# Optimization experiments

Measured on AMD Instinct MI355X. Metric: run time of the kernel, lower is better.

Reference implementation:

```python
import jax, jax.numpy as jnp
import numpy as np

N_NODES = 100000
N_EDGES = 400000
N_GRAPHS = 5000
F_IN = 64
H = 128
OUT = 1
N_LAYERS = 3  # gat_conv + 2 atom_gats
NEG_SLOPE = 0.01


def _gat_conv(x_src, x_dst, src, dst, W, a_src, a_dst, b, num_dst):
    """PyG GATConv, heads=1, add_self_loops=False, negative_slope=0.01.

    x_src: [Ns, Fin], x_dst: [Nd, Fin]; src/dst: [E] int; W: [Fin, H];
    a_src, a_dst, b: [H]. Returns [Nd, H].
    """
    hs = x_src @ W                      # [Ns, H]
    hd = x_dst @ W                      # [Nd, H]
    as_n = hs @ a_src                   # [Ns]
    ad_n = hd @ a_dst                   # [Nd]
    e = jax.nn.leaky_relu(as_n[src] + ad_n[dst], NEG_SLOPE)  # [E]
    # segment softmax over destination nodes
    seg_max = jax.ops.segment_max(e, dst, num_segments=num_dst)
    seg_max = jnp.where(jnp.isfinite(seg_max), seg_max, 0.0)
    ex = jnp.exp(e - seg_max[dst])
    denom = jax.ops.segment_sum(ex, dst, num_segments=num_dst) + 1e-16
    alpha = ex / denom[dst]             # [E]
    out = jax.ops.segment_sum(alpha[:, None] * hs[src], dst, num_segments=num_dst)
    return out + b


def setup_inputs() -> dict:
    key = jax.random.key(0)
    ks = jax.random.split(key, 16)
    x = jax.random.normal(ks[0], (N_NODES, F_IN), dtype=jnp.float32)
    edge_index = jax.random.randint(ks[1], (2, N_EDGES), 0, N_NODES, dtype=jnp.int64)
    batch = jnp.sort(jax.random.randint(ks[2], (N_NODES,), 0, N_GRAPHS, dtype=jnp.int64))
    s_in = 1.0 / np.sqrt(F_IN)
    s_h = 1.0 / np.sqrt(H)
    W1 = jax.random.uniform(ks[3], (F_IN, H), jnp.float32, -s_in, s_in)
    b1 = jax.random.uniform(ks[4], (H,), jnp.float32, -s_in, s_in)
    gW = jax.random.normal(ks[5], (N_LAYERS, H, H), jnp.float32) * s_h
    g_asrc = jax.random.normal(ks[6], (N_LAYERS, H), jnp.float32) * s_h
    g_adst = jax.random.normal(ks[7], (N_LAYERS, H), jnp.float32) * s_h
    g_b = jnp.zeros((N_LAYERS, H), jnp.float32)
    mW = jax.random.normal(ks[8], (H, H), jnp.float32) * s_h
    m_asrc = jax.random.normal(ks[9], (H,), jnp.float32) * s_h
    m_adst = jax.random.normal(ks[10], (H,), jnp.float32) * s_h
    m_b = jnp.zeros((H,), jnp.float32)
    W2 = jax.random.uniform(ks[11], (H, OUT), jnp.float32, -s_h, s_h)
    b2 = jax.random.uniform(ks[12], (OUT,), jnp.float32, -s_h, s_h)
    return {"x": x, "edge_index": edge_index, "batch": batch,
            "W1": W1, "b1": b1, "gW": gW, "g_asrc": g_asrc,
            "g_adst": g_adst, "g_b": g_b, "mW": mW, "m_asrc": m_asrc,
            "m_adst": m_adst, "m_b": m_b, "W2": W2, "b2": b2}


def reference(x, edge_index, batch, W1, b1, gW, g_asrc, g_adst, g_b,
              mW, m_asrc, m_adst, m_b, W2, b2):
    src, dst = edge_index[0], edge_index[1]
    h = jax.nn.leaky_relu(x @ W1 + b1, NEG_SLOPE)            # lin1 + leaky_relu_
    for i in range(N_LAYERS):                                 # gat_conv + atom_gats
        h = jax.nn.elu(_gat_conv(h, h, src, dst, gW[i], g_asrc[i],
                                 g_adst[i], g_b[i], N_NODES))
    # global readout: node -> graph bipartite GAT
    pooled = jax.nn.relu(jax.ops.segment_sum(h, batch, num_segments=N_GRAPHS))
    row = jnp.arange(N_NODES)
    out = jax.nn.elu(_gat_conv(h, pooled, row, batch, mW, m_asrc,
                               m_adst, m_b, N_GRAPHS))
    return out @ W2 + b2                                      # [N_GRAPHS, OUT]
```

## Files before the change

### kernel.cpp

```cpp
#include <hip/hip_runtime.h>
#include <hip/hip_fp16.h>
#include <math.h>
#include <stdint.h>

#define DEV __device__ __forceinline__

using f32x4 = __attribute__((ext_vector_type(4))) float;
using half8 = __attribute__((ext_vector_type(8))) _Float16;
typedef union { uint4 u; half8 h; } u4h8;

DEV float lrelu(float x){ return x > 0.f ? x : 0.01f*x; }
DEV float elu1(float x){ return x > 0.f ? x : __expf(x)-1.f; }

DEV int lower_bound_i(const int* __restrict__ a, int n, int key){
  int lo = 0, hi = n;
  while (lo < hi){ int mid = (lo+hi)>>1; if (a[mid] < key) lo = mid+1; else hi = mid; }
  return lo;
}

DEV void wsplit(float v, unsigned short* __restrict__ H, unsigned short* __restrict__ L, size_t o){
  __half h = __float2half_rn(v);
  float lo = (v - __half2float(h)) * 1024.f;
  H[o] = __half_as_ushort(h);
  L[o] = __half_as_ushort(__float2half_rn(lo));
}

__global__ void wprep_all(const float* __restrict__ W1, const float* __restrict__ gW,
    const float* __restrict__ mW,
    unsigned short* __restrict__ w1h, unsigned short* __restrict__ w1l,
    unsigned short* __restrict__ gwh, unsigned short* __restrict__ gwl,
    unsigned short* __restrict__ mwh, unsigned short* __restrict__ mwl,
    int* __restrict__ deg, unsigned long long* __restrict__ bstat,
    int* __restrict__ bctr, int Nn, int nG, int nscan)
{
  int i = blockIdx.x*256 + threadIdx.x;
  if (i < Nn) deg[i] = 0;
  if (i < nscan) bstat[i] = 0ull;
  if (i == 0) *bctr = 0;
  if (i < 8192){
    int k = i >> 7, n = i & 127;
    wsplit(W1[i], w1h, w1l, (size_t)n*64 + k);
  }
  if (i < nG){
    int mat = i >> 14; int rem = i & 16383;
    int k = rem >> 7, n = rem & 127;
    wsplit(gW[i], gwh, gwl, (size_t)mat*16384 + (size_t)n*128 + k);
  }
  if (i < 16384){
    int k = i >> 7, n = i & 127;
    wsplit(mW[i], mwh, mwl, (size_t)n*128 + k);
  }
}

__global__ __launch_bounds__(256, 3) void gemm_lin1(
    const float* __restrict__ X, const unsigned short* __restrict__ Wt_hi,
    const unsigned short* __restrict__ Wt_lo, const float* __restrict__ bias,
    unsigned short* __restrict__ Ch, int M)
{
  const int tid = threadIdx.x;
  const int lane = tid & 63;
  const int wv = tid >> 6;
  const int ml = lane & 15;
  const int kg = lane >> 4;
  const int R0 = blockIdx.x * 64;

  __shared__ uint32_t sA[2][1024];
  __shared__ float sC[4][32][36];

  const unsigned short* bhp[2];
  const unsigned short* blp[2];
  #pragma unroll
  for (int nt = 0; nt < 2; ++nt){
    int n = wv*32 + nt*16 + ml;
    bhp[nt] = Wt_hi + (size_t)n*64 + kg*8;
    blp[nt] = Wt_lo + (size_t)n*64 + kg*8;
  }

  {
    int row = tid >> 2, kq = tid & 3;
    int gr = R0 + row; gr = gr < M ? gr : M-1;
    const float4* xp = (const float4*)(X + (size_t)gr*64 + kq*16);
    int sub = kq >> 1;
    #pragma unroll
    for (int i = 0; i < 4; ++i){
      float4 v = xp[i];
      __half2 h0 = __floats2half2_rn(v.x, v.y);
      __half2 h1 = __floats2half2_rn(v.z, v.w);
      int slot = (kq & 1)*2 + (i >> 1);
      int slot_s = slot ^ ((row >> 1) & 3);
      int byte = row*64 + slot_s*16 + (i & 1)*8;
      *(uint2*)((char*)&sA[sub][0] + byte) = make_uint2(*(uint32_t*)&h0, *(uint32_t*)&h1);
    }
  }
  __syncthreads();

  f32x4 accH[4][2], accL[4][2];
  #pragma unroll
  for (int mt = 0; mt < 4; ++mt)
    #pragma unroll
    for (int nt = 0; nt < 2; ++nt){
      accH[mt][nt] = (f32x4){0.f,0.f,0.f,0.f};
      accL[mt][nt] = (f32x4){0.f,0.f,0.f,0.f};
    }

  #pragma unroll
  for (int sc = 0; sc < 2; ++sc){
    u4h8 bh[2], bl[2];
    #pragma unroll
    for (int nt = 0; nt < 2; ++nt){
      bh[nt].u = *(const uint4*)(bhp[nt] + sc*32);
      bl[nt].u = *(const uint4*)(blp[nt] + sc*32);
    }
    const char* buf = (const char*)&sA[sc][0];
    #pragma unroll
    for (int mt = 0; mt < 4; ++mt){
      int row = mt*16 + ml;
      int ba = row*64 + ((kg ^ ((row >> 1) & 3)) * 16);
      u4h8 A_;
      A_.u = *(const uint4*)(buf + ba);
      #pragma unroll
      for (int nt = 0; nt < 2; ++nt){
        accH[mt][nt] = __builtin_amdgcn_mfma_f32_16x16x32_f16(A_.h, bh[nt].h, accH[mt][nt], 0, 0, 0);
        accL[mt][nt] = __builtin_amdgcn_mfma_f32_16x16x32_f16(A_.h, bl[nt].h, accL[mt][nt], 0, 0, 0);
      }
    }
  }

  float bv[2] = { bias[wv*32 + ml], bias[wv*32 + 16 + ml] };
  #pragma unroll
  for (int p = 0; p < 2; ++p){
    #pragma unroll
    for (int mh = 0; mh < 2; ++mh){
      int mt = p*2 + mh;
      #pragma unroll
      for (int nt = 0; nt < 2; ++nt){
        #pragma unroll
        for (int r = 0; r < 4; ++r){
          float v = accH[mt][nt][r] + accL[mt][nt][r] * 9.765625e-4f;
          v = lrelu(v + bv[nt]);
          sC[wv][mh*16 + kg*4 + r][nt*16 + ml] = v;
        }
      }
    }
    __syncthreads();
    #pragma unroll
    for (int j = 0; j < 4; ++j){
      int row_l = j*8 + (lane >> 3);
      int c4 = (lane & 7) * 4;
      int grow = R0 + p*32 + row_l;
      if (grow < M){
        float4 v = *(const float4*)&sC[wv][row_l][c4];
        int gcol = wv*32 + c4;
        __half2 h0 = __floats2half2_rn(v.x, v.y);
        __half2 h1 = __floats2half2_rn(v.z, v.w);
        *(uint2*)(Ch + (size_t)grow*128 + gcol) = make_uint2(*(uint32_t*)&h0, *(uint32_t*)&h1);
      }
    }
    __syncthreads();
  }
}

template<int OUTMODE, bool DOTA, bool DOTB>
__global__ __launch_bounds__(256, 3) void gemm_mfma(
    const unsigned short* __restrict__ Ah, const unsigned short* __restrict__ Wt_hi,
    const unsigned short* __restrict__ Wt_lo,
    const float* __restrict__ va, const float* __restrict__ vb,
    unsigned short* __restrict__ Ch,
    float* __restrict__ outa, float* __restrict__ outb, int M)
{
  constexpr int K = 128;
  const int tid = threadIdx.x;
  const int lane = tid & 63;
  const int wv = tid >> 6;
  const int ml = lane & 15;
  const int kg = lane >> 4;
  const int R0 = blockIdx.x * 64;

  __shared__ uint32_t sA[4][1024];
  __shared__ float sC[4][32][36];
  __shared__ float sd[4][64][2];

  const unsigned short* bhp[2];
  const unsigned short* blp[2];
  #pragma unroll
  for (int nt = 0; nt < 2; ++nt){
    int n = wv*32 + nt*16 + ml;
    bhp[nt] = Wt_hi + (size_t)n*K + kg*8;
    blp[nt] = Wt_lo + (size_t)n*K + kg*8;
  }

  auto STAGE = [&](int ch){
    #pragma unroll
    for (int j = 0; j < 2; ++j){
      int sc = ch*2 + j;
      int o = tid*16;
      int row = o >> 6;
      int t = (o >> 4) & 3;
      int gr = R0 + row; gr = gr < M ? gr : M-1;
      int jj = t ^ ((row >> 1) & 3);
      const char* src = (const char*)(Ah + (size_t)gr*K + sc*32 + jj*8);
      char* dst = (char*)(&sA[(ch & 1)*2 + j][0]) + wv*1024;
      __builtin_amdgcn_global_load_lds(
          (const __attribute__((address_space(1))) void*)src,
          (__attribute__((address_space(3))) void*)dst, 16, 0, 0);
    }
  };

  f32x4 accH[4][2], accL[4][2];
  #pragma unroll
  for (int mt = 0; mt < 4; ++mt)
    #pragma unroll
    for (int nt = 0; nt < 2; ++nt){
      accH[mt][nt] = (f32x4){0.f,0.f,0.f,0.f};
      accL[mt][nt] = (f32x4){0.f,0.f,0.f,0.f};
    }

  STAGE(0);
  u4h8 bh[2][2], bl[2][2];
  #pragma unroll
  for (int j = 0; j < 2; ++j)
    #pragma unroll
    for (int nt = 0; nt < 2; ++nt){
      bh[j][nt].u = *(const uint4*)(bhp[nt] + j*32);
      bl[j][nt].u = *(const uint4*)(blp[nt] + j*32);
    }
  __syncthreads();

  #pragma unroll
  for (int ch = 0; ch < 2; ++ch){
    u4h8 bhN[2][2], blN[2][2];
    if (ch == 0){
      STAGE(1);
      #pragma unroll
      for (int j = 0; j < 2; ++j)
        #pragma unroll
        for (int nt = 0; nt < 2; ++nt){
          bhN[j][nt].u = *(const uint4*)(bhp[nt] + (2 + j)*32);
          blN[j][nt].u = *(const uint4*)(blp[nt] + (2 + j)*32);
        }
    }
    #pragma unroll
    for (int js = 0; js < 2; ++js){
      const char* buf = (const char*)&sA[(ch & 1)*2 + js][0];
      #pragma unroll
      for (int mt = 0; mt < 4; ++mt){
        int row = mt*16 + ml;
        int ba = row*64 + ((kg ^ ((row >> 1) & 3)) * 16);
        u4h8 A_;
        A_.u = *(const uint4*)(buf + ba);
        #pragma unroll
        for (int nt = 0; nt < 2; ++nt){
          accH[mt][nt] = __builtin_amdgcn_mfma_f32_16x16x32_f16(A_.h, bh[js][nt].h, accH[mt][nt], 0, 0, 0);
          accL[mt][nt] = __builtin_amdgcn_mfma_f32_16x16x32_f16(A_.h, bl[js][nt].h, accL[mt][nt], 0, 0, 0);
        }
      }
    }
    __syncthreads();
    if (ch == 0){
      #pragma unroll
      for (int j = 0; j < 2; ++j)
        #pragma unroll
        for (int nt = 0; nt < 2; ++nt){ bh[j][nt] = bhN[j][nt]; bl[j][nt] = blN[j][nt]; }
    }
  }

  #pragma unroll
  for (int mt = 0; mt < 4; ++mt)
    #pragma unroll
    for (int nt = 0; nt < 2; ++nt)
      accH[mt][nt] = accH[mt][nt] + accL[mt][nt] * 9.765625e-4f;

  if constexpr (DOTA || DOTB){
    float vaL[2] = {0.f,0.f}, vbL[2] = {0.f,0.f};
    if constexpr (DOTA){ vaL[0] = va[wv*32 + ml]; vaL[1] = va[wv*32 + 16 + ml]; }
    if constexpr (DOTB){ vbL[0] = vb[wv*32 + ml]; vbL[1] = vb[wv*32 + 16 + ml]; }
    #pragma unroll
    for (int mt = 0; mt < 4; ++mt){
      #pragma unroll
      for (int r = 0; r < 4; ++r){
        float pa = 0.f, pb = 0.f;
        #pragma unroll
        for (int nt = 0; nt < 2; ++nt){
          float v = accH[mt][nt][r];
          if constexpr (DOTA) pa = fmaf(v, vaL[nt], pa);
          if constexpr (DOTB) pb = fmaf(v, vbL[nt], pb);
        }
        #pragma unroll
        for (int o = 8; o; o >>= 1){
          if constexpr (DOTA) pa += __shfl_xor(pa, o, 64);
          if constexpr (DOTB) pb += __shfl_xor(pb, o, 64);
        }
        if (ml == 0){
          int rl = mt*16 + kg*4 + r;
          sd[wv][rl][0] = pa;
          sd[wv][rl][1] = pb;
        }
      }
    }
    __syncthreads();
    if (tid < 64){
      int row = R0 + tid;
      if (row < M){
        if constexpr (DOTA)
          outa[row] = sd[0][tid][0] + sd[1][tid][0] + sd[2][tid][0] + sd[3][tid][0];
        if constexpr (DOTB)
          outb[row] = sd[0][tid][1] + sd[1][tid][1] + sd[2][tid][1] + sd[3][tid][1];
      }
    }
  }

  if constexpr (OUTMODE == 2){
    if constexpr (DOTA || DOTB) __syncthreads();
    #pragma unroll
    for (int p = 0; p < 2; ++p){
      #pragma unroll
      for (int mh = 0; mh < 2; ++mh){
        int mt = p*2 + mh;
        #pragma unroll
        for (int nt = 0; nt < 2; ++nt){
          #pragma unroll
          for (int r = 0; r < 4; ++r)
            sC[wv][mh*16 + kg*4 + r][nt*16 + ml] = accH[mt][nt][r];
        }
      }
      __syncthreads();
      #pragma unroll
      for (int j = 0; j < 4; ++j){
        int row_l = j*8 + (lane >> 3);
        int c4 = (lane & 7) * 4;
        int grow = R0 + p*32 + row_l;
        if (grow < M){
          float4 v = *(const float4*)&sC[wv][row_l][c4];
          int gcol = wv*32 + c4;
          __half2 h0 = __floats2half2_rn(v.x, v.y);
          __half2 h1 = __floats2half2_rn(v.z, v.w);
          *(uint2*)(Ch + (size_t)grow*128 + gcol) = make_uint2(*(uint32_t*)&h0, *(uint32_t*)&h1);
        }
      }
      __syncthreads();
    }
  }
}

__global__ void hist_k(const int* __restrict__ dstv, int* __restrict__ deg, int E){
  int e = blockIdx.x*256 + threadIdx.x;
  if (e < E) atomicAdd(&deg[dstv[e]], 1);
}

__global__ void scan_onepass(const int* __restrict__ deg, int* __restrict__ rp,
    int* __restrict__ cur, unsigned long long* __restrict__ bstat,
    int* __restrict__ bctr, int n, int E)
{
  __shared__ int sbid;
  __shared__ int swsum[4];
  __shared__ int sprev;
  if (threadIdx.x == 0) sbid = atomicAdd(bctr, 1);
  __syncthreads();
  const int bid = sbid;
  int i = bid*256 + threadIdx.x;
  int lane = threadIdx.x & 63, wv = threadIdx.x >> 6;
  int v = (i < n) ? deg[i] : 0;
  int inc = v;
  #pragma unroll
  for (int o = 1; o < 64; o <<= 1){
    int u = __shfl_up(inc, o, 64);
    if (lane >= o) inc += u;
  }
  if (lane == 63) swsum[wv] = inc;
  __syncthreads();
  if (threadIdx.x == 0){
    int bsum = swsum[0]+swsum[1]+swsum[2]+swsum[3];
    atomicExch(&bstat[bid], (1ull << 62) | (unsigned long long)(unsigned)bsum);
    int prev = 0;
    for (int j = bid - 1; j >= 0; --j){
      unsigned long long s;
      do { s = atomicAdd(&bstat[j], 0ull); } while ((s >> 62) == 0);
      prev += (int)(s & 0xffffffffull);
      if ((s >> 62) == 2) break;
    }
    atomicExch(&bstat[bid], (2ull << 62) | (unsigned long long)(unsigned)(prev + bsum));
    sprev = prev;
  }
  __syncthreads();
  int woff = sprev;
  for (int wq = 0; wq < wv; ++wq) woff += swsum[wq];
  int excl = woff + inc - v;
  if (i < n){ rp[i] = excl; cur[i] = excl; }
  if (bid == 0 && threadIdx.x == 0) rp[n] = E;
}

__global__ void scatter_k(const int* __restrict__ srcv, const int* __restrict__ dstv,
                          int* __restrict__ cur, int* __restrict__ ssorted, int E){
  int e = blockIdx.x*256 + threadIdx.x;
  if (e < E){
    int p = atomicAdd(&cur[dstv[e]], 1);
    ssorted[p] = srcv[e];
  }
}

__global__ __launch_bounds__(256) void gat_agg(const int* __restrict__ ssorted,
    const int* __restrict__ rp,
    const float* __restrict__ asn, const float* __restrict__ adn,
    const uint4* __restrict__ hsv, const float* __restrict__ bias,
    uint4* __restrict__ outv, int Nn)
{
  const int lane = threadIdx.x & 63;
  const int wv = threadIdx.x >> 6;
  const int l16 = lane & 15;
  const int gbase = lane & 48;
  const int d = blockIdx.x*16 + wv*4 + (lane >> 4);
  const bool valid = d < Nn;
  const int dc = valid ? d : Nn-1;
  const int lo = rp[dc], hi = rp[dc+1];
  const int deg = valid ? (hi - lo) : 0;
  const float ad = adn[dc];
  float acc[8] = {0.f,0.f,0.f,0.f,0.f,0.f,0.f,0.f};

  const bool fast = (deg <= 16);
  const int fdeg = fast ? deg : 0;
  int mdeg = fdeg;
  mdeg = max(mdeg, __shfl_xor(mdeg, 16, 64));
  mdeg = max(mdeg, __shfl_xor(mdeg, 32, 64));

  int sid = 0; float lg = -1e30f;
  if (l16 < fdeg){
    sid = ssorted[lo + l16];
    lg = lrelu(asn[sid] + ad);
  }
  float m = lg;
  m = fmaxf(m, __shfl_xor(m, 8, 64));
  m = fmaxf(m, __shfl_xor(m, 4, 64));
  m = fmaxf(m, __shfl_xor(m, 2, 64));
  m = fmaxf(m, __shfl_xor(m, 1, 64));
  float p = (l16 < fdeg) ? __expf(lg - m) : 0.f;
  float s = p;
  s += __shfl_xor(s, 8, 64);
  s += __shfl_xor(s, 4, 64);
  s += __shfl_xor(s, 2, 64);
  s += __shfl_xor(s, 1, 64);
  float alpha = p * (1.f / (s + 1e-16f));

  for (int i = 0; i < mdeg; ++i){
    if (i < fdeg){
      float al = __shfl(alpha, gbase + i, 64);
      int sd = __shfl(sid, gbase + i, 64);
      uint4 v = hsv[(size_t)sd*16 + l16];
      float2 f0 = __half22float2(*(__half2*)&v.x);
      float2 f1 = __half22float2(*(__half2*)&v.y);
      float2 f2 = __half22float2(*(__half2*)&v.z);
      float2 f3 = __half22float2(*(__half2*)&v.w);
      acc[0] = fmaf(al, f0.x, acc[0]); acc[1] = fmaf(al, f0.y, acc[1]);
      acc[2] = fmaf(al, f1.x, acc[2]); acc[3] = fmaf(al, f1.y, acc[3]);
      acc[4] = fmaf(al, f2.x, acc[4]); acc[5] = fmaf(al, f2.y, acc[5]);
      acc[6] = fmaf(al, f3.x, acc[6]); acc[7] = fmaf(al, f3.y, acc[7]);
    }
  }

  if (!fast){
    float mg = -1e30f;
    for (int e = l16; e < deg; e += 16){
      int sd = ssorted[lo + e];
      mg = fmaxf(mg, lrelu(asn[sd] + ad));
    }
    mg = fmaxf(mg, __shfl_xor(mg, 8, 64));
    mg = fmaxf(mg, __shfl_xor(mg, 4, 64));
    mg = fmaxf(mg, __shfl_xor(mg, 2, 64));
    mg = fmaxf(mg, __shfl_xor(mg, 1, 64));
    float sg = 0.f;
    for (int e = l16; e < deg; e += 16){
      int sd = ssorted[lo + e];
      sg += __expf(lrelu(asn[sd] + ad) - mg);
    }
    sg += __shfl_xor(sg, 8, 64);
    sg += __shfl_xor(sg, 4, 64);
    sg += __shfl_xor(sg, 2, 64);
    sg += __shfl_xor(sg, 1, 64);
    float inv = 1.f / (sg + 1e-16f);
    for (int e = 0; e < deg; ++e){
      int sd = ssorted[lo + e];
      float a = __expf(lrelu(asn[sd] + ad) - mg) * inv;
      uint4 v = hsv[(size_t)sd*16 + l16];
      float2 f0 = __half22float2(*(__half2*)&v.x);
      float2 f1 = __half22float2(*(__half2*)&v.y);
      float2 f2 = __half22float2(*(__half2*)&v.z);
      float2 f3 = __half22float2(*(__half2*)&v.w);
      acc[0] = fmaf(a, f0.x, acc[0]); acc[1] = fmaf(a, f0.y, acc[1]);
      acc[2] = fmaf(a, f1.x, acc[2]); acc[3] = fmaf(a, f1.y, acc[3]);
      acc[4] = fmaf(a, f2.x, acc[4]); acc[5] = fmaf(a, f2.y, acc[5]);
      acc[6] = fmaf(a, f3.x, acc[6]); acc[7] = fmaf(a, f3.y, acc[7]);
    }
  }

  if (valid){
    float4 b0 = ((const float4*)bias)[l16*2];
    float4 b1 = ((const float4*)bias)[l16*2 + 1];
    __half2 h0 = __floats2half2_rn(elu1(acc[0]+b0.x), elu1(acc[1]+b0.y));
    __half2 h1 = __floats2half2_rn(elu1(acc[2]+b0.z), elu1(acc[3]+b0.w));
    __half2 h2 = __floats2half2_rn(elu1(acc[4]+b1.x), elu1(acc[5]+b1.y));
    __half2 h3 = __floats2half2_rn(elu1(acc[6]+b1.z), elu1(acc[7]+b1.w));
    outv[(size_t)d*16 + l16] = make_uint4(*(uint32_t*)&h0, *(uint32_t*)&h1,
                                          *(uint32_t*)&h2, *(uint32_t*)&h3);
  }
}

__global__ __launch_bounds__(256) void pool_relu(const uint4* __restrict__ hv,
    const int* __restrict__ batch, uint4* __restrict__ ptail, int Nn, int G)
{
  const int lane = threadIdx.x & 63;
  const int wv = threadIdx.x >> 6;
  const int l16 = lane & 15;
  const int g = blockIdx.x*16 + wv*4 + (lane >> 4);
  if (g >= G) return;
  const int lo = lower_bound_i(batch, Nn, g);
  const int hi = lower_bound_i(batch, Nn, g + 1);
  float acc[8] = {0.f,0.f,0.f,0.f,0.f,0.f,0.f,0.f};
  for (int i = lo; i < hi; ++i){
    uint4 v = hv[(size_t)i*16 + l16];
    float2 f0 = __half22float2(*(__half2*)&v.x);
    float2 f1 = __half22float2(*(__half2*)&v.y);
    float2 f2 = __half22float2(*(__half2*)&v.z);
    float2 f3 = __half22float2(*(__half2*)&v.w);
    acc[0] += f0.x; acc[1] += f0.y; acc[2] += f1.x; acc[3] += f1.y;
    acc[4] += f2.x; acc[5] += f2.y; acc[6] += f3.x; acc[7] += f3.y;
  }
  __half2 h0 = __floats2half2_rn(fmaxf(acc[0],0.f), fmaxf(acc[1],0.f));
  __half2 h1 = __floats2half2_rn(fmaxf(acc[2],0.f), fmaxf(acc[3],0.f));
  __half2 h2 = __floats2half2_rn(fmaxf(acc[4],0.f), fmaxf(acc[5],0.f));
  __half2 h3 = __floats2half2_rn(fmaxf(acc[6],0.f), fmaxf(acc[7],0.f));
  ptail[(size_t)g*16 + l16] = make_uint4(*(uint32_t*)&h0, *(uint32_t*)&h1,
                                         *(uint32_t*)&h2, *(uint32_t*)&h3);
}

__global__ __launch_bounds__(128) void mol_agg(const float* __restrict__ as2,
    const float* __restrict__ ad2, const unsigned short* __restrict__ hs2,
    const int* __restrict__ batch, const float* __restrict__ bias,
    const float* __restrict__ W2, const float* __restrict__ b2,
    float* __restrict__ out, int Nn)
{
  const int g = blockIdx.x;
  const int c = threadIdx.x;
  __shared__ int sb[2];
  __shared__ float red[2];
  if (c < 2) sb[c] = lower_bound_i(batch, Nn, g + c);
  __syncthreads();
  const int lo = sb[0], hi = sb[1];
  const float ad = ad2[g];

  float mt = -1e30f;
  for (int i = lo + c; i < hi; i += 128) mt = fmaxf(mt, lrelu(as2[i] + ad));
  #pragma unroll
  for (int o = 32; o; o >>= 1) mt = fmaxf(mt, __shfl_xor(mt, o, 64));
  if ((c & 63) == 0) red[c >> 6] = mt;
  __syncthreads();
  const float m = fmaxf(red[0], red[1]);

  float st = 0.f;
  for (int i = lo + c; i < hi; i += 128) st += __expf(lrelu(as2[i] + ad) - m);
  #pragma unroll
  for (int o = 32; o; o >>= 1) st += __shfl_xor(st, o, 64);
  __syncthreads();
  if ((c & 63) == 0) red[c >> 6] = st;
  __syncthreads();
  const float inv = 1.f / (red[0] + red[1] + 1e-16f);

  float acc = 0.f;
  for (int i = lo; i < hi; ++i){
    float wgt = __expf(lrelu(as2[i] + ad) - m) * inv;
    acc = fmaf(wgt, __half2float(__ushort_as_half(hs2[(size_t)i*128 + c])), acc);
  }
  float v = elu1(acc + bias[c]);

  float r = v * W2[c];
  #pragma unroll
  for (int o = 32; o; o >>= 1) r += __shfl_xor(r, o, 64);
  __syncthreads();
  if ((c & 63) == 0) red[c >> 6] = r;
  __syncthreads();
  if (c == 0) out[g] = red[0] + red[1] + b2[0];
}

extern "C" void kernel_launch(void* const* d_in, const int* in_sizes, int n_in,
                              void* d_out, int out_size, void* d_ws, size_t ws_size,
                              hipStream_t stream)
{
  const float* x      = (const float*)d_in[0];
  const int*   ei     = (const int*)  d_in[1];
  const int*   batch  = (const int*)  d_in[2];
  const float* W1     = (const float*)d_in[3];
  const float* b1     = (const float*)d_in[4];
  const float* gW     = (const float*)d_in[5];
  const float* g_asrc = (const float*)d_in[6];
  const float* g_adst = (const float*)d_in[7];
  const float* g_b    = (const float*)d_in[8];
  const float* mW     = (const float*)d_in[9];
  const float* m_asrc = (const float*)d_in[10];
  const float* m_adst = (const float*)d_in[11];
  const float* m_b    = (const float*)d_in[12];
  const float* W2     = (const float*)d_in[13];
  const float* b2     = (const float*)d_in[14];

  const int Nn = in_sizes[0] / 64;
  const int E  = in_sizes[1] / 2;
  const int G  = out_size;
  const int NL = in_sizes[5] / (128*128);
  const int M2 = Nn + G;
  const int* srcv = ei;
  const int* dstv = ei + E;

  char* w = (char*)d_ws;
  unsigned short* h16 = (unsigned short*)w; w += (size_t)(M2+64)*128*2;
  unsigned short* hsR = (unsigned short*)w; w += (size_t)(M2+64)*128*2;
  float* asO      = (float*)w; w += (size_t)(M2+64)*4;
  float* adO      = (float*)w; w += (size_t)(M2+64)*4;
  int*   deg      = (int*)w;   w += (size_t)Nn*4;
  int*   rp       = (int*)w;   w += (size_t)(Nn+64)*4;
  int*   cur      = (int*)w;   w += (size_t)Nn*4;
  int*   ssorted  = (int*)w;   w += (size_t)E*4;
  unsigned long long* bstat = (unsigned long long*)w; w += 512*8;
  int*   bctr     = (int*)w;   w += 64;
  unsigned short* w1h = (unsigned short*)w; w += 64*128*2;
  unsigned short* w1l = (unsigned short*)w; w += 64*128*2;
  unsigned short* gwh = (unsigned short*)w; w += (size_t)NL*128*128*2;
  unsigned short* gwl = (unsigned short*)w; w += (size_t)NL*128*128*2;
  unsigned short* mwh = (unsigned short*)w; w += 128*128*2;
  unsigned short* mwl = (unsigned short*)w; w += 128*128*2;

  const int nscan = (Nn + 255)/256;
  const int nrt = (Nn + 63)/64;
  const int mrt = (M2 + 63)/64;

  wprep_all<<<nscan, 256, 0, stream>>>(W1, gW, mW, w1h, w1l, gwh, gwl, mwh, mwl,
                                       deg, bstat, bctr, Nn, NL*16384, nscan);

  hist_k<<<(E+255)/256, 256, 0, stream>>>(dstv, deg, E);
  scan_onepass<<<nscan, 256, 0, stream>>>(deg, rp, cur, bstat, bctr, Nn, E);
  scatter_k<<<(E+255)/256, 256, 0, stream>>>(srcv, dstv, cur, ssorted, E);

  gemm_lin1<<<nrt, 256, 0, stream>>>(x, w1h, w1l, b1, h16, Nn);

  for (int l = 0; l < NL; ++l){
    gemm_mfma<2, true, true><<<nrt, 256, 0, stream>>>(
        h16, gwh + (size_t)l*128*128, gwl + (size_t)l*128*128,
        g_asrc + l*128, g_adst + l*128, hsR, asO, adO, Nn);
    gat_agg<<<(Nn+15)/16, 256, 0, stream>>>(ssorted, rp, asO, adO,
        (const uint4*)hsR, g_b + l*128, (uint4*)h16, Nn);
  }

  pool_relu<<<(G+15)/16, 256, 0, stream>>>((const uint4*)h16, batch,
      (uint4*)(h16 + (size_t)Nn*128), Nn, G);
  gemm_mfma<2, true, true><<<mrt, 256, 0, stream>>>(
      h16, mwh, mwl, m_asrc, m_adst, hsR, asO, adO, M2);
  mol_agg<<<G, 128, 0, stream>>>(asO, adO + Nn, hsR, batch, m_b, W2, b2, (float*)d_out, Nn);
}
```

Measured before the change: 318.1 us.

## Alias GEMM LDS buffers, raise occupancy, and batch neighbor gathers by four

The MFMA GEMM now shares one LDS buffer between the A staging tiles and the output staging tile. It raises the launch-bounds occupancy hint from 3 to 4 blocks per SM. It loads the W fragments for each k-step just before use instead of prefetching them, which cuts register pressure but may expose global-load latency. The GAT aggregation loop now handles four neighbors per iteration, issuing four row gathers before the FMAs to increase memory-level parallelism; padded slots contribute zero weight.

```diff
diff --git a/kernel.cpp b/kernel.cpp
--- a/kernel.cpp
+++ b/kernel.cpp
@@ -161,7 +161,7 @@
 }
 
 template<int OUTMODE, bool DOTA, bool DOTB>
-__global__ __launch_bounds__(256, 3) void gemm_mfma(
+__global__ __launch_bounds__(256, 4) void gemm_mfma(
     const unsigned short* __restrict__ Ah, const unsigned short* __restrict__ Wt_hi,
     const unsigned short* __restrict__ Wt_lo,
     const float* __restrict__ va, const float* __restrict__ vb,
@@ -176,9 +176,11 @@
   const int kg = lane >> 4;
   const int R0 = blockIdx.x * 64;
 
-  __shared__ uint32_t sA[4][1024];
-  __shared__ float sC[4][32][36];
+  __shared__ char smem[18432];
   __shared__ float sd[4][64][2];
+  uint32_t* sA = (uint32_t*)smem;
+  typedef float sC_t[32][36];
+  sC_t* sC = (sC_t*)smem;
 
   const unsigned short* bhp[2];
   const unsigned short* blp[2];
@@ -199,7 +201,7 @@
       int gr = R0 + row; gr = gr < M ? gr : M-1;
       int jj = t ^ ((row >> 1) & 3);
       const char* src = (const char*)(Ah + (size_t)gr*K + sc*32 + jj*8);
-      char* dst = (char*)(&sA[(ch & 1)*2 + j][0]) + wv*1024;
+      char* dst = (char*)sA + ((ch & 1)*2 + j)*4096 + wv*1024;
       __builtin_amdgcn_global_load_lds(
           (const __attribute__((address_space(1))) void*)src,
           (__attribute__((address_space(3))) void*)dst, 16, 0, 0);
@@ -216,32 +218,21 @@
     }
 
   STAGE(0);
-  u4h8 bh[2][2], bl[2][2];
-  #pragma unroll
-  for (int j = 0; j < 2; ++j)
-    #pragma unroll
-    for (int nt = 0; nt < 2; ++nt){
-      bh[j][nt].u = *(const uint4*)(bhp[nt] + j*32);
-      bl[j][nt].u = *(const uint4*)(blp[nt] + j*32);
-    }
   __syncthreads();
 
   #pragma unroll
   for (int ch = 0; ch < 2; ++ch){
-    u4h8 bhN[2][2], blN[2][2];
-    if (ch == 0){
-      STAGE(1);
+    if (ch == 0) STAGE(1);
+    #pragma unroll
+    for (int js = 0; js < 2; ++js){
+      int sc = ch*2 + js;
+      u4h8 bh[2], bl[2];
       #pragma unroll
-      for (int j = 0; j < 2; ++j)
-        #pragma unroll
-        for (int nt = 0; nt < 2; ++nt){
-          bhN[j][nt].u = *(const uint4*)(bhp[nt] + (2 + j)*32);
-          blN[j][nt].u = *(const uint4*)(blp[nt] + (2 + j)*32);
-        }
-    }
-    #pragma unroll
-    for (int js = 0; js < 2; ++js){
-      const char* buf = (const char*)&sA[(ch & 1)*2 + js][0];
+      for (int nt = 0; nt < 2; ++nt){
+        bh[nt].u = *(const uint4*)(bhp[nt] + sc*32);
+        bl[nt].u = *(const uint4*)(blp[nt] + sc*32);
+      }
+      const char* buf = (const char*)sA + ((ch & 1)*2 + js)*4096;
       #pragma unroll
       for (int mt = 0; mt < 4; ++mt){
         int row = mt*16 + ml;
@@ -250,18 +241,12 @@
         A_.u = *(const uint4*)(buf + ba);
         #pragma unroll
         for (int nt = 0; nt < 2; ++nt){
-          accH[mt][nt] = __builtin_amdgcn_mfma_f32_16x16x32_f16(A_.h, bh[js][nt].h, accH[mt][nt], 0, 0, 0);
-          accL[mt][nt] = __builtin_amdgcn_mfma_f32_16x16x32_f16(A_.h, bl[js][nt].h, accL[mt][nt], 0, 0, 0);
+          accH[mt][nt] = __builtin_amdgcn_mfma_f32_16x16x32_f16(A_.h, bh[nt].h, accH[mt][nt], 0, 0, 0);
+          accL[mt][nt] = __builtin_amdgcn_mfma_f32_16x16x32_f16(A_.h, bl[nt].h, accL[mt][nt], 0, 0, 0);
         }
       }
     }
     __syncthreads();
-    if (ch == 0){
-      #pragma unroll
-      for (int j = 0; j < 2; ++j)
-        #pragma unroll
-        for (int nt = 0; nt < 2; ++nt){ bh[j][nt] = bhN[j][nt]; bl[j][nt] = blN[j][nt]; }
-    }
   }
 
   #pragma unroll
@@ -307,10 +292,10 @@
           outb[row] = sd[0][tid][1] + sd[1][tid][1] + sd[2][tid][1] + sd[3][tid][1];
       }
     }
+    __syncthreads();
   }
 
   if constexpr (OUTMODE == 2){
-    if constexpr (DOTA || DOTB) __syncthreads();
     #pragma unroll
     for (int p = 0; p < 2; ++p){
       #pragma unroll
@@ -421,6 +406,7 @@
   int mdeg = fdeg;
   mdeg = max(mdeg, __shfl_xor(mdeg, 16, 64));
   mdeg = max(mdeg, __shfl_xor(mdeg, 32, 64));
+  const int nb = (mdeg + 3) & ~3;
 
   int sid = 0; float lg = -1e30f;
   if (l16 < fdeg){
@@ -440,19 +426,26 @@
   s += __shfl_xor(s, 1, 64);
   float alpha = p * (1.f / (s + 1e-16f));
 
-  for (int i = 0; i < mdeg; ++i){
-    if (i < fdeg){
-      float al = __shfl(alpha, gbase + i, 64);
-      int sd = __shfl(sid, gbase + i, 64);
-      uint4 v = hsv[(size_t)sd*16 + l16];
-      float2 f0 = __half22float2(*(__half2*)&v.x);
-      float2 f1 = __half22float2(*(__half2*)&v.y);
-      float2 f2 = __half22float2(*(__half2*)&v.z);
-      float2 f3 = __half22float2(*(__half2*)&v.w);
-      acc[0] = fmaf(al, f0.x, acc[0]); acc[1] = fmaf(al, f0.y, acc[1]);
-      acc[2] = fmaf(al, f1.x, acc[2]); acc[3] = fmaf(al, f1.y, acc[3]);
-      acc[4] = fmaf(al, f2.x, acc[4]); acc[5] = fmaf(al, f2.y, acc[5]);
-      acc[6] = fmaf(al, f3.x, acc[6]); acc[7] = fmaf(al, f3.y, acc[7]);
+  for (int i = 0; i < nb; i += 4){
+    float al[4]; int sd[4]; uint4 v[4];
+    #pragma unroll
+    for (int j = 0; j < 4; ++j){
+      al[j] = __shfl(alpha, gbase + i + j, 64);
+      sd[j] = __shfl(sid, gbase + i + j, 64);
+    }
+    #pragma unroll
+    for (int j = 0; j < 4; ++j)
+      v[j] = hsv[(size_t)sd[j]*16 + l16];
+    #pragma unroll
+    for (int j = 0; j < 4; ++j){
+      float2 f0 = __half22float2(*(__half2*)&v[j].x);
+      float2 f1 = __half22float2(*(__half2*)&v[j].y);
+      float2 f2 = __half22float2(*(__half2*)&v[j].z);
+      float2 f3 = __half22float2(*(__half2*)&v[j].w);
+      acc[0] = fmaf(al[j], f0.x, acc[0]); acc[1] = fmaf(al[j], f0.y, acc[1]);
+      acc[2] = fmaf(al[j], f1.x, acc[2]); acc[3] = fmaf(al[j], f1.y, acc[3]);
+      acc[4] = fmaf(al[j], f2.x, acc[4]); acc[5] = fmaf(al[j], f2.y, acc[5]);
+      acc[6] = fmaf(al[j], f3.x, acc[6]); acc[7] = fmaf(al[j], f3.y, acc[7]);
     }
   }
 
```

After: 302.7 us. -4.8%, faster.
